# Optimization experiments

Measured on AMD Instinct MI355X. Metric: run time of the kernel, lower is better.

The kernel has to match this reference:

```python
import jax, jax.numpy as jnp
import numpy as np

B, C, L, H = 8, 256, 2048, 4
HD = C // H
LIP = 1.0
EPS = 1e-12
LN_EPS = 1e-5


def setup_inputs() -> dict:
    key = jax.random.key(0)
    ks = jax.random.split(key, 9)
    s = 0.05  # weight init scale
    inp = {"x_in": jax.random.normal(ks[0], (B, C, L), jnp.float32)}
    for i, p in enumerate(["q", "k", "v"]):
        k1, k2 = jax.random.split(ks[1 + i])
        inp[f"{p}_w1"] = jax.random.normal(k1, (C, C), jnp.float32) * s
        inp[f"{p}_b1"] = jnp.zeros((C,), jnp.float32)
        inp[f"{p}_w2"] = jax.random.normal(k2, (C, C), jnp.float32) * s
        inp[f"{p}_b2"] = jnp.zeros((C,), jnp.float32)
    inp["o_w"] = jax.random.normal(ks[4], (C, C), jnp.float32) * s
    inp["o_b"] = jnp.zeros((C,), jnp.float32)
    inp["ln_g"] = jnp.ones((C,), jnp.float32)
    inp["ln_b"] = jnp.zeros((C,), jnp.float32)
    return inp


def _mlp(x, w1, b1, w2, b2):
    # Linear -> exact GELU -> Linear (matches nn.GELU default, erf form)
    return jax.nn.gelu(x @ w1 + b1, approximate=False) @ w2 + b2


def reference(x_in, q_w1, q_b1, q_w2, q_b2, k_w1, k_b1, k_w2, k_b2,
              v_w1, v_b1, v_w2, v_b2, o_w, o_b, ln_g, ln_b):
    x = x_in.transpose(0, 2, 1)  # [B, L, C]

    def heads(t):
        return t.reshape(B, L, H, HD).transpose(0, 2, 1, 3)  # [B, H, L, HD]

    Q = heads(_mlp(x, q_w1, q_b1, q_w2, q_b2))
    K = heads(_mlp(x, k_w1, k_b1, k_w2, k_b2))
    V = heads(_mlp(x, v_w1, v_b1, v_w2, v_b2))

    scores = jnp.einsum('bhqd,bhkd->bhqk', Q, K) / jnp.sqrt(jnp.float32(HD))
    # Lipschitz rescale: divide each score row by its L2 norm
    row_norm = jnp.sqrt(jnp.sum(scores * scores, axis=-1, keepdims=True))
    scores = scores / (row_norm * LIP + EPS)
    attn = jax.nn.softmax(scores, axis=-1)

    out = jnp.einsum('bhqk,bhkd->bhqd', attn, V)  # [B, H, L, HD]
    out = out.transpose(0, 2, 1, 3).reshape(B, L, C)
    out = out @ o_w + o_b

    # LayerNorm over channel dim (torch LN: biased variance, eps=1e-5)
    mu = jnp.mean(out, axis=-1, keepdims=True)
    var = jnp.mean((out - mu) ** 2, axis=-1, keepdims=True)
    out = (out - mu) / jnp.sqrt(var + LN_EPS) * ln_g + ln_b

    out = out.transpose(0, 2, 1)  # [B, C, L]
    return jax.nn.elu(out) + x_in
```

## Files before the change

kernel.cpp:

```cpp
#include <hip/hip_runtime.h>
#include <hip/hip_bf16.h>
#include <cstdint>
#include <cstddef>

#define B_  8
#define C_  256
#define L_  2048
#define H_  4
#define HD_ 64

using short8v = __attribute__((ext_vector_type(8))) short;
using f32x4   = __attribute__((ext_vector_type(4))) float;

__device__ __forceinline__ float gelu_exact(float v) {
  return 0.5f * v * (1.0f + erff(v * 0.70710678118654752440f));
}

__device__ __forceinline__ short f2bf(float v) {
  __hip_bfloat16 h = __float2bfloat16(v);
  return *reinterpret_cast<short*>(&h);
}

__device__ __forceinline__ float bf2f(short s) {
  __hip_bfloat16 h = *reinterpret_cast<__hip_bfloat16*>(&s);
  return __bfloat162float(h);
}

__device__ __forceinline__ void fma16(float (&acc)[4][4], const float4 a, const float4 b) {
  acc[0][0] += a.x * b.x; acc[0][1] += a.x * b.y; acc[0][2] += a.x * b.z; acc[0][3] += a.x * b.w;
  acc[1][0] += a.y * b.x; acc[1][1] += a.y * b.y; acc[1][2] += a.y * b.z; acc[1][3] += a.y * b.w;
  acc[2][0] += a.z * b.x; acc[2][1] += a.z * b.y; acc[2][2] += a.z * b.z; acc[2][3] += a.z * b.w;
  acc[3][0] += a.w * b.x; acc[3][1] += a.w * b.y; acc[3][2] += a.w * b.z; acc[3][3] += a.w * b.w;
}

__global__ __launch_bounds__(256) void k_transpose(const float* __restrict__ x,
                                                   float* __restrict__ Xr) {
  __shared__ float t[32][33];
  const int l0 = blockIdx.x * 32;
  const int c0 = blockIdx.y * 32;
  const int b  = blockIdx.z;
  const int tx = threadIdx.x;
  const int ty = threadIdx.y;
  const float* xp  = x  + (size_t)b * C_ * L_;
  float*       xrp = Xr + (size_t)b * L_ * C_;
#pragma unroll
  for (int i = 0; i < 32; i += 8)
    t[ty + i][tx] = xp[(size_t)(c0 + ty + i) * L_ + (l0 + tx)];
  __syncthreads();
#pragma unroll
  for (int i = 0; i < 32; i += 8)
    xrp[(size_t)(l0 + ty + i) * C_ + (c0 + tx)] = t[tx][ty + i];
}

__global__ __launch_bounds__(256) void k_packw(
    const float* __restrict__ w0, const float* __restrict__ w1,
    const float* __restrict__ w2, const float* __restrict__ w3,
    const float* __restrict__ w4, const float* __restrict__ w5,
    const float* __restrict__ w6,
    short* __restrict__ hi, short* __restrict__ lo) {
  const float* Ws[7] = {w0, w1, w2, w3, w4, w5, w6};
  const int wi = blockIdx.z;
  const float* W = Ws[wi];
  __shared__ float T[32][33];
  const int k0 = blockIdx.x * 32, n0 = blockIdx.y * 32;
  const int tx = threadIdx.x & 31, ty = threadIdx.x >> 5;
#pragma unroll
  for (int i = 0; i < 32; i += 8)
    T[ty + i][tx] = W[(size_t)(k0 + ty + i) * 256 + n0 + tx];
  __syncthreads();
  short* ho = hi + (size_t)wi * 65536;
  short* lp = lo + (size_t)wi * 65536;
#pragma unroll
  for (int i = 0; i < 32; i += 8) {
    float v = T[tx][ty + i];
    short h = f2bf(v);
    float r = v - bf2f(h);
    ho[(size_t)(n0 + ty + i) * 256 + k0 + tx] = h;
    lp[(size_t)(n0 + ty + i) * 256 + k0 + tx] = f2bf(r);
  }
}

__global__ __launch_bounds__(256, 3) void k_gemm_s(
    const float* __restrict__ A, const short* __restrict__ Wth,
    const short* __restrict__ Wtl, const float* __restrict__ bias,
    float* __restrict__ Cout, int actGelu) {
  __shared__ short Ah[2][64 * 32], Al[2][64 * 32];
  __shared__ short Bh[2][128 * 32], Bl[2][128 * 32];
  const int tid  = threadIdx.x;
  const int lane = tid & 63;
  const int w    = tid >> 6;
  const int wm = w & 1, wn = w >> 1;
  const int m0 = blockIdx.x * 64;
  const int n0 = blockIdx.y * 128;
  const int l15 = lane & 15, lg = lane >> 4;

  const int ar  = tid >> 2;
  const int ag  = tid & 3;
  const int br  = tid >> 1;
  const int bg0 = (tid & 1) * 2;

  float4 fA0, fA1;
  short8v rBh0, rBh1, rBl0, rBl1;
  auto gload = [&](int ks) {
    const float* ap = &A[(size_t)(m0 + ar) * 256 + ks * 32 + ag * 8];
    fA0 = *reinterpret_cast<const float4*>(ap);
    fA1 = *reinterpret_cast<const float4*>(ap + 4);
    const short* bph = &Wth[(size_t)(n0 + br) * 256 + ks * 32 + bg0 * 8];
    const short* bpl = &Wtl[(size_t)(n0 + br) * 256 + ks * 32 + bg0 * 8];
    rBh0 = *reinterpret_cast<const short8v*>(bph);
    rBh1 = *reinterpret_cast<const short8v*>(bph + 8);
    rBl0 = *reinterpret_cast<const short8v*>(bpl);
    rBl1 = *reinterpret_cast<const short8v*>(bpl + 8);
  };
  auto lwrite = [&](int buf) {
    float av[8] = {fA0.x, fA0.y, fA0.z, fA0.w, fA1.x, fA1.y, fA1.z, fA1.w};
    short8v h8, l8;
#pragma unroll
    for (int i = 0; i < 8; ++i) {
      short h = f2bf(av[i]);
      h8[i] = h;
      l8[i] = f2bf(av[i] - bf2f(h));
    }
    const int gA = ag ^ (ar & 3);
    *reinterpret_cast<short8v*>(&Ah[buf][ar * 32 + gA * 8]) = h8;
    *reinterpret_cast<short8v*>(&Al[buf][ar * 32 + gA * 8]) = l8;
    const int g0 = bg0 ^ (br & 3);
    const int g1 = (bg0 + 1) ^ (br & 3);
    *reinterpret_cast<short8v*>(&Bh[buf][br * 32 + g0 * 8]) = rBh0;
    *reinterpret_cast<short8v*>(&Bh[buf][br * 32 + g1 * 8]) = rBh1;
    *reinterpret_cast<short8v*>(&Bl[buf][br * 32 + g0 * 8]) = rBl0;
    *reinterpret_cast<short8v*>(&Bl[buf][br * 32 + g1 * 8]) = rBl1;
  };

  const f32x4 z4 = {0.f, 0.f, 0.f, 0.f};
  f32x4 acc[2][4];
#pragma unroll
  for (int s = 0; s < 2; ++s)
#pragma unroll
    for (int nt = 0; nt < 4; ++nt) acc[s][nt] = z4;

  gload(0);
  lwrite(0);
  __syncthreads();

  for (int ks = 0; ks < 8; ++ks) {
    const int cur = ks & 1;
    if (ks < 7) gload(ks + 1);
    short8v a_h[2], a_l[2];
#pragma unroll
    for (int s = 0; s < 2; ++s) {
      const int m = wm * 32 + s * 16 + l15;
      const int g = lg ^ (m & 3);
      a_h[s] = *reinterpret_cast<const short8v*>(&Ah[cur][m * 32 + g * 8]);
      a_l[s] = *reinterpret_cast<const short8v*>(&Al[cur][m * 32 + g * 8]);
    }
#pragma unroll
    for (int nt = 0; nt < 4; ++nt) {
      const int n = wn * 64 + nt * 16 + l15;
      const int g = lg ^ (n & 3);
      short8v b_h = *reinterpret_cast<const short8v*>(&Bh[cur][n * 32 + g * 8]);
      short8v b_l = *reinterpret_cast<const short8v*>(&Bl[cur][n * 32 + g * 8]);
#pragma unroll
      for (int s = 0; s < 2; ++s) {
        acc[s][nt] = __builtin_amdgcn_mfma_f32_16x16x32_bf16(a_h[s], b_h, acc[s][nt], 0, 0, 0);
        acc[s][nt] = __builtin_amdgcn_mfma_f32_16x16x32_bf16(a_h[s], b_l, acc[s][nt], 0, 0, 0);
        acc[s][nt] = __builtin_amdgcn_mfma_f32_16x16x32_bf16(a_l[s], b_h, acc[s][nt], 0, 0, 0);
      }
    }
    if (ks < 7) lwrite(cur ^ 1);
    __syncthreads();
  }

#pragma unroll
  for (int nt = 0; nt < 4; ++nt) {
    const int col = n0 + wn * 64 + nt * 16 + l15;
    const float bv = bias[col];
#pragma unroll
    for (int s = 0; s < 2; ++s)
#pragma unroll
      for (int r = 0; r < 4; ++r) {
        const int row = m0 + wm * 32 + s * 16 + lg * 4 + r;
        float v = acc[s][nt][r] + bv;
        if (actGelu) v = gelu_exact(v);
        Cout[(size_t)row * 256 + col] = v;
      }
  }
}

__global__ __launch_bounds__(256) void k_gram(const float* __restrict__ Kg,
                                              float* __restrict__ Gp) {
  __shared__ float Ks[64][68];
  const int tid = threadIdx.x;
  const int tm = tid >> 4;
  const int tn = tid & 15;
  const int chunk = blockIdx.x;
  const int h = blockIdx.y;
  const int b = blockIdx.z;
  const size_t base = (size_t)b * L_ * C_ + (size_t)h * HD_ + (size_t)chunk * 256 * C_;
  const int lr = tid >> 2;
  const int lf = tid & 3;
  float acc[4][4] = {};
  for (int st = 0; st < 4; ++st) {
    __syncthreads();
#pragma unroll
    for (int i = 0; i < 4; ++i) {
      int fg = lf * 4 + i;
      float4 v = *reinterpret_cast<const float4*>(&Kg[base + (size_t)(st * 64 + lr) * C_ + fg * 4]);
      *reinterpret_cast<float4*>(&Ks[lr][fg * 4]) = v;
    }
    __syncthreads();
#pragma unroll 16
    for (int r = 0; r < 64; ++r) {
      float4 a  = *reinterpret_cast<const float4*>(&Ks[r][tm << 2]);
      float4 b2 = *reinterpret_cast<const float4*>(&Ks[r][tn << 2]);
      fma16(acc, a, b2);
    }
  }
  const int bh = b * H_ + h;
  float* gp = Gp + ((size_t)bh * 8 + chunk) * 4096;
#pragma unroll
  for (int i = 0; i < 4; ++i)
    *reinterpret_cast<float4*>(&gp[((tm << 2) + i) * 64 + (tn << 2)]) =
        make_float4(acc[i][0], acc[i][1], acc[i][2], acc[i][3]);
}

__global__ __launch_bounds__(256) void k_gram_reduce(const float* __restrict__ Gp,
                                                     float* __restrict__ G) {
  const int bh = blockIdx.x;
  const int tid = threadIdx.x;
  for (int t = tid; t < 4096; t += 256) {
    float s = 0.f;
#pragma unroll
    for (int c = 0; c < 8; ++c) s += Gp[((size_t)bh * 8 + c) * 4096 + t];
    G[(size_t)bh * 4096 + t] = s;
  }
}

__global__ __launch_bounds__(256) void k_scale(const float* __restrict__ Qg,
                                               const float* __restrict__ Gm,
                                               float* __restrict__ Scl) {
  __shared__ float QsT[64][68];
  __shared__ float Gs[64][68];
  const int tid = threadIdx.x;
  const int tm = tid >> 4;
  const int tn = tid & 15;
  const int q0 = blockIdx.x * 64;
  const int h  = blockIdx.y;
  const int b  = blockIdx.z;
  const int bh = b * H_ + h;
  const size_t base = (size_t)b * L_ * C_ + (size_t)h * HD_;
  const int lr = tid >> 2;
  const int lf = tid & 3;
#pragma unroll
  for (int i = 0; i < 4; ++i) {
    int fg = lf * 4 + i;
    float4 v = *reinterpret_cast<const float4*>(&Qg[base + (size_t)(q0 + lr) * C_ + fg * 4]);
    QsT[fg * 4 + 0][lr] = v.x;
    QsT[fg * 4 + 1][lr] = v.y;
    QsT[fg * 4 + 2][lr] = v.z;
    QsT[fg * 4 + 3][lr] = v.w;
    float4 g = *reinterpret_cast<const float4*>(&Gm[(size_t)bh * 4096 + lr * 64 + fg * 4]);
    *reinterpret_cast<float4*>(&Gs[lr][fg * 4]) = g;
  }
  __syncthreads();
  float t4[4][4] = {};
#pragma unroll 16
  for (int e = 0; e < 64; ++e) {
    float4 a  = *reinterpret_cast<const float4*>(&QsT[e][tm << 2]);
    float4 b2 = *reinterpret_cast<const float4*>(&Gs[e][tn << 2]);
    fma16(t4, a, b2);
  }
  float r2[4];
#pragma unroll
  for (int i = 0; i < 4; ++i) {
    r2[i] = t4[i][0] * QsT[(tn << 2) + 0][(tm << 2) + i]
          + t4[i][1] * QsT[(tn << 2) + 1][(tm << 2) + i]
          + t4[i][2] * QsT[(tn << 2) + 2][(tm << 2) + i]
          + t4[i][3] * QsT[(tn << 2) + 3][(tm << 2) + i];
#pragma unroll
    for (int o = 8; o; o >>= 1) r2[i] += __shfl_xor(r2[i], o);
  }
  if (tn == 0) {
#pragma unroll
    for (int i = 0; i < 4; ++i) {
      float rr = fmaxf(r2[i], 0.f);
      Scl[(size_t)bh * L_ + q0 + (tm << 2) + i] = 1.0f / (sqrtf(rr) + 8e-12f);
    }
  }
}

__global__ __launch_bounds__(256) void k_pack_qk(const float* __restrict__ Qf,
                                                 const float* __restrict__ Kf,
                                                 short* __restrict__ Qh,
                                                 short* __restrict__ Kh) {
  const int blk = blockIdx.x;
  const int tid = threadIdx.x;
#pragma unroll
  for (int i = 0; i < 16; ++i) {
    int idx = tid + 256 * i;
    int row = idx >> 6;
    int c4  = idx & 63;
    int R = blk * 64 + row;
    int b = R >> 11, l = R & 2047;
    int h = c4 >> 4, d4 = c4 & 15;
    size_t o = ((size_t)(b * H_ + h) * L_ + l) * HD_ + d4 * 4;
    float4 q = *reinterpret_cast<const float4*>(&Qf[(size_t)R * C_ + c4 * 4]);
    float4 k = *reinterpret_cast<const float4*>(&Kf[(size_t)R * C_ + c4 * 4]);
    short4 qs, ks;
    qs.x = f2bf(q.x); qs.y = f2bf(q.y); qs.z = f2bf(q.z); qs.w = f2bf(q.w);
    ks.x = f2bf(k.x); ks.y = f2bf(k.y); ks.z = f2bf(k.z); ks.w = f2bf(k.w);
    *reinterpret_cast<short4*>(&Qh[o]) = qs;
    *reinterpret_cast<short4*>(&Kh[o]) = ks;
  }
}

__global__ __launch_bounds__(256) void k_packt_v(const float* __restrict__ Vf,
                                                 short* __restrict__ Vt) {
  __shared__ float T[64][65];
  const int lt = blockIdx.x;
  const int h = blockIdx.y, b = blockIdx.z;
  const int bh = b * H_ + h;
  const int tid = threadIdx.x;
#pragma unroll
  for (int i = 0; i < 4; ++i) {
    int idx = tid + 256 * i;
    int l = idx >> 4;
    int c4 = idx & 15;
    float4 v = *reinterpret_cast<const float4*>(
        &Vf[(size_t)(b * L_ + lt * 64 + l) * C_ + h * HD_ + c4 * 4]);
    T[l][c4 * 4 + 0] = v.x;
    T[l][c4 * 4 + 1] = v.y;
    T[l][c4 * 4 + 2] = v.z;
    T[l][c4 * 4 + 3] = v.w;
  }
  __syncthreads();
  const int d  = tid >> 2;
  const int ls = (tid & 3) * 16;
#pragma unroll
  for (int i = 0; i < 4; ++i) {
    int l = ls + i * 4;
    short4 s;
    s.x = f2bf(T[l + 0][d]);
    s.y = f2bf(T[l + 1][d]);
    s.z = f2bf(T[l + 2][d]);
    s.w = f2bf(T[l + 3][d]);
    *reinterpret_cast<short4*>(&Vt[((size_t)bh * HD_ + d) * L_ + lt * 64 + l]) = s;
  }
}

__device__ __forceinline__ int swz(int r, int c) {
  return (r * 64 + c) ^ ((r & 7) << 3);
}

__global__ __launch_bounds__(256) void k_attn_mfma(
    const short* __restrict__ Qh, const short* __restrict__ Kh,
    const short* __restrict__ Vt, const float* __restrict__ Scl,
    float* __restrict__ AO) {
  __shared__ short Ks[2][64 * 64];
  __shared__ short Vs[2][64 * 64];
  __shared__ short Ps[4][32 * 64];
  const int tid  = threadIdx.x;
  const int lane = tid & 63;
  const int w    = tid >> 6;
  const int h = blockIdx.y, b = blockIdx.z;
  const int bh = b * H_ + h;
  const size_t hb = (size_t)bh * L_ * HD_;
  const int q0 = blockIdx.x * 128 + w * 32;
  const int l15 = lane & 15;
  const int lg  = lane >> 4;
  const int srow = tid >> 3;
  const int sseg = tid & 7;

  short8v aq[2][2];
#pragma unroll
  for (int sub = 0; sub < 2; ++sub)
#pragma unroll
    for (int ch = 0; ch < 2; ++ch)
      aq[sub][ch] = *reinterpret_cast<const short8v*>(
          &Qh[hb + (size_t)(q0 + sub * 16 + l15) * HD_ + ch * 32 + lg * 8]);

  float sr[2][4];
#pragma unroll
  for (int sub = 0; sub < 2; ++sub)
#pragma unroll
    for (int r = 0; r < 4; ++r)
      sr[sub][r] = Scl[(size_t)bh * L_ + q0 + sub * 16 + lg * 4 + r];

  short8v stK0, stK1, stV0, stV1;
  auto stage_load = [&](int kt) {
    stK0 = *reinterpret_cast<const short8v*>(&Kh[hb + (size_t)(kt * 64 + srow) * HD_ + sseg * 8]);
    stK1 = *reinterpret_cast<const short8v*>(&Kh[hb + (size_t)(kt * 64 + 32 + srow) * HD_ + sseg * 8]);
    stV0 = *reinterpret_cast<const short8v*>(&Vt[hb + (size_t)srow * L_ + kt * 64 + sseg * 8]);
    stV1 = *reinterpret_cast<const short8v*>(&Vt[hb + (size_t)(32 + srow) * L_ + kt * 64 + sseg * 8]);
  };
  auto stage_write = [&](int buf) {
    *reinterpret_cast<short8v*>(&Ks[buf][swz(srow, sseg * 8)]) = stK0;
    *reinterpret_cast<short8v*>(&Ks[buf][swz(32 + srow, sseg * 8)]) = stK1;
    *reinterpret_cast<short8v*>(&Vs[buf][swz(srow, sseg * 8)]) = stV0;
    *reinterpret_cast<short8v*>(&Vs[buf][swz(32 + srow, sseg * 8)]) = stV1;
  };

  const f32x4 z4 = {0.f, 0.f, 0.f, 0.f};
  float lsum[2][4] = {};
  f32x4 oacc[2][4];
#pragma unroll
  for (int s = 0; s < 2; ++s)
#pragma unroll
    for (int d = 0; d < 4; ++d) oacc[s][d] = z4;

  stage_load(0);
  stage_write(0);
  __syncthreads();

  for (int kt = 0; kt < 32; ++kt) {
    const int cur = kt & 1;
    if (kt < 31) stage_load(kt + 1);

    f32x4 sacc[2][4];
#pragma unroll
    for (int s = 0; s < 2; ++s)
#pragma unroll
      for (int nt = 0; nt < 4; ++nt) sacc[s][nt] = z4;
#pragma unroll
    for (int nt = 0; nt < 4; ++nt) {
      short8v kb0 = *reinterpret_cast<const short8v*>(&Ks[cur][swz(nt * 16 + l15, lg * 8)]);
      short8v kb1 = *reinterpret_cast<const short8v*>(&Ks[cur][swz(nt * 16 + l15, 32 + lg * 8)]);
#pragma unroll
      for (int sub = 0; sub < 2; ++sub) {
        sacc[sub][nt] = __builtin_amdgcn_mfma_f32_16x16x32_bf16(aq[sub][0], kb0, sacc[sub][nt], 0, 0, 0);
        sacc[sub][nt] = __builtin_amdgcn_mfma_f32_16x16x32_bf16(aq[sub][1], kb1, sacc[sub][nt], 0, 0, 0);
      }
    }

#pragma unroll
    for (int sub = 0; sub < 2; ++sub)
#pragma unroll
      for (int nt = 0; nt < 4; ++nt)
#pragma unroll
        for (int r = 0; r < 4; ++r) {
          float p = __expf(sacc[sub][nt][r] * sr[sub][r]);
          lsum[sub][r] += p;
          Ps[w][swz(sub * 16 + lg * 4 + r, nt * 16 + l15)] = f2bf(p);
        }
    asm volatile("s_waitcnt lgkmcnt(0)");
    __builtin_amdgcn_sched_barrier(0);

    short8v pa[2][2];
#pragma unroll
    for (int sub = 0; sub < 2; ++sub) {
      pa[sub][0] = *reinterpret_cast<const short8v*>(&Ps[w][swz(sub * 16 + l15, lg * 8)]);
      pa[sub][1] = *reinterpret_cast<const short8v*>(&Ps[w][swz(sub * 16 + l15, 32 + lg * 8)]);
    }
#pragma unroll
    for (int dt = 0; dt < 4; ++dt) {
      short8v vb0 = *reinterpret_cast<const short8v*>(&Vs[cur][swz(dt * 16 + l15, lg * 8)]);
      short8v vb1 = *reinterpret_cast<const short8v*>(&Vs[cur][swz(dt * 16 + l15, 32 + lg * 8)]);
#pragma unroll
      for (int sub = 0; sub < 2; ++sub) {
        oacc[sub][dt] = __builtin_amdgcn_mfma_f32_16x16x32_bf16(pa[sub][0], vb0, oacc[sub][dt], 0, 0, 0);
        oacc[sub][dt] = __builtin_amdgcn_mfma_f32_16x16x32_bf16(pa[sub][1], vb1, oacc[sub][dt], 0, 0, 0);
      }
    }
    __syncthreads();
    if (kt < 31) {
      stage_write(cur ^ 1);
      __syncthreads();
    }
  }

#pragma unroll
  for (int sub = 0; sub < 2; ++sub)
#pragma unroll
    for (int r = 0; r < 4; ++r) {
#pragma unroll
      for (int o = 8; o; o >>= 1) lsum[sub][r] += __shfl_xor(lsum[sub][r], o);
    }

#pragma unroll
  for (int sub = 0; sub < 2; ++sub)
#pragma unroll
    for (int r = 0; r < 4; ++r) {
      const float inv = 1.0f / lsum[sub][r];
      const int q = q0 + sub * 16 + lg * 4 + r;
#pragma unroll
      for (int dt = 0; dt < 4; ++dt)
        AO[(size_t)(b * L_ + q) * C_ + h * HD_ + dt * 16 + l15] = oacc[sub][dt][r] * inv;
    }
}

__global__ __launch_bounds__(256) void k_ln(const float* __restrict__ PO,
                                            const float* __restrict__ x,
                                            const float* __restrict__ g,
                                            const float* __restrict__ bta,
                                            float* __restrict__ out) {
  __shared__ float buf[32][257];
  __shared__ float mu_s[32], rs_s[32];
  __shared__ float gs[256], bs[256];
  const int b  = blockIdx.y;
  const int l0 = blockIdx.x * 32;
  const int tid = threadIdx.x;
  gs[tid] = g[tid];
  bs[tid] = bta[tid];
#pragma unroll 8
  for (int r = 0; r < 32; ++r)
    buf[r][tid] = PO[((size_t)b * L_ + l0 + r) * C_ + tid];
  __syncthreads();
  {
    const int r  = tid >> 3;
    const int c0 = tid & 7;
    float s1 = 0.f;
#pragma unroll
    for (int i = 0; i < 32; ++i) s1 += buf[r][c0 + (i << 3)];
#pragma unroll
    for (int o = 4; o; o >>= 1) s1 += __shfl_xor(s1, o);
    float mu = s1 * (1.0f / 256.0f);
    float s2 = 0.f;
#pragma unroll
    for (int i = 0; i < 32; ++i) {
      float dv = buf[r][c0 + (i << 3)] - mu;
      s2 += dv * dv;
    }
#pragma unroll
    for (int o = 4; o; o >>= 1) s2 += __shfl_xor(s2, o);
    if (c0 == 0) {
      mu_s[r] = mu;
      rs_s[r] = rsqrtf(s2 * (1.0f / 256.0f) + 1e-5f);
    }
  }
  __syncthreads();
  const int tl = tid & 31;
  const int tc = tid >> 5;
  const float mu = mu_s[tl];
  const float rs = rs_s[tl];
#pragma unroll 8
  for (int c = tc; c < 256; c += 8) {
    float y = (buf[tl][c] - mu) * rs * gs[c] + bs[c];
    float e = (y > 0.f) ? y : (__expf(y) - 1.0f);
    size_t idx = ((size_t)b * C_ + c) * L_ + l0 + tl;
    out[idx] = e + x[idx];
  }
}

extern "C" void kernel_launch(void* const* d_in, const int* in_sizes, int n_in,
                              void* d_out, int out_size, void* d_ws, size_t ws_size,
                              hipStream_t stream) {
  const float* x_in = (const float*)d_in[0];
  const float* q_w1 = (const float*)d_in[1];
  const float* q_b1 = (const float*)d_in[2];
  const float* q_w2 = (const float*)d_in[3];
  const float* q_b2 = (const float*)d_in[4];
  const float* k_w1 = (const float*)d_in[5];
  const float* k_b1 = (const float*)d_in[6];
  const float* k_w2 = (const float*)d_in[7];
  const float* k_b2 = (const float*)d_in[8];
  const float* v_w1 = (const float*)d_in[9];
  const float* v_b1 = (const float*)d_in[10];
  const float* v_w2 = (const float*)d_in[11];
  const float* v_b2 = (const float*)d_in[12];
  const float* o_w  = (const float*)d_in[13];
  const float* o_b  = (const float*)d_in[14];
  const float* ln_g = (const float*)d_in[15];
  const float* ln_b = (const float*)d_in[16];
  float* out = (float*)d_out;
  float* ws  = (float*)d_ws;

  const size_t NB = (size_t)B_ * L_ * C_;
  float* Xr = ws;
  float* Hb = ws + NB;
  float* Qb = ws + 2 * NB;
  float* Kb = ws + 3 * NB;
  float* Gp = ws + 4 * NB;
  float* G  = Gp + (size_t)32 * 8 * 4096;
  float* Scl = G + (size_t)32 * 4096;
  short* Vt  = (short*)(Scl + (size_t)32 * 2048);
  short* Whi = Vt + (size_t)32 * HD_ * L_;
  short* Wlo = Whi + (size_t)7 * 65536;
  float* Vb = Xr;
  short* Qh = (short*)Hb;
  short* Kh = (short*)(Hb + NB / 2);
  float* AO = Kb;
  float* PO = Qb;

  dim3 ggrid(B_ * L_ / 64, C_ / 128);

  k_packw<<<dim3(8, 8, 7), 256, 0, stream>>>(q_w1, q_w2, k_w1, k_w2, v_w1, v_w2, o_w, Whi, Wlo);
  k_transpose<<<dim3(L_ / 32, C_ / 32, B_), dim3(32, 8), 0, stream>>>(x_in, Xr);

  const size_t WN = 65536;
  k_gemm_s<<<ggrid, 256, 0, stream>>>(Xr, Whi + 0 * WN, Wlo + 0 * WN, q_b1, Hb, 1);
  k_gemm_s<<<ggrid, 256, 0, stream>>>(Hb, Whi + 1 * WN, Wlo + 1 * WN, q_b2, Qb, 0);
  k_gemm_s<<<ggrid, 256, 0, stream>>>(Xr, Whi + 2 * WN, Wlo + 2 * WN, k_b1, Hb, 1);
  k_gemm_s<<<ggrid, 256, 0, stream>>>(Hb, Whi + 3 * WN, Wlo + 3 * WN, k_b2, Kb, 0);
  k_gemm_s<<<ggrid, 256, 0, stream>>>(Xr, Whi + 4 * WN, Wlo + 4 * WN, v_b1, Hb, 1);
  k_gemm_s<<<ggrid, 256, 0, stream>>>(Hb, Whi + 5 * WN, Wlo + 5 * WN, v_b2, Vb, 0);

  k_gram<<<dim3(8, H_, B_), 256, 0, stream>>>(Kb, Gp);
  k_gram_reduce<<<dim3(32), 256, 0, stream>>>(Gp, G);
  k_scale<<<dim3(L_ / 64, H_, B_), 256, 0, stream>>>(Qb, G, Scl);

  k_pack_qk<<<dim3(B_ * L_ / 64), 256, 0, stream>>>(Qb, Kb, Qh, Kh);
  k_packt_v<<<dim3(L_ / 64, H_, B_), 256, 0, stream>>>(Vb, Vt);

  k_attn_mfma<<<dim3(L_ / 128, H_, B_), 256, 0, stream>>>(Qh, Kh, Vt, Scl, AO);

  k_gemm_s<<<ggrid, 256, 0, stream>>>(AO, Whi + 6 * WN, Wlo + 6 * WN, o_b, PO, 0);

  k_ln<<<dim3(L_ / 32, B_), 256, 0, stream>>>(PO, x_in, ln_g, ln_b, out);
}
```

Before: 318.3 us.

## Store intermediates as pre-split bf16 hi/lo pairs and drop the separate Q/K packing pass

```diff
diff --git a/kernel.cpp b/kernel.cpp
--- a/kernel.cpp
+++ b/kernel.cpp
@@ -33,23 +33,28 @@
   acc[3][0] += a.w * b.x; acc[3][1] += a.w * b.y; acc[3][2] += a.w * b.z; acc[3][3] += a.w * b.w;
 }
 
-__global__ __launch_bounds__(256) void k_transpose(const float* __restrict__ x,
-                                                   float* __restrict__ Xr) {
+__global__ __launch_bounds__(256) void k_transpose_s(const float* __restrict__ x,
+                                                     short* __restrict__ Xh,
+                                                     short* __restrict__ Xl) {
   __shared__ float t[32][33];
   const int l0 = blockIdx.x * 32;
   const int c0 = blockIdx.y * 32;
   const int b  = blockIdx.z;
   const int tx = threadIdx.x;
   const int ty = threadIdx.y;
-  const float* xp  = x  + (size_t)b * C_ * L_;
-  float*       xrp = Xr + (size_t)b * L_ * C_;
+  const float* xp = x + (size_t)b * C_ * L_;
 #pragma unroll
   for (int i = 0; i < 32; i += 8)
     t[ty + i][tx] = xp[(size_t)(c0 + ty + i) * L_ + (l0 + tx)];
   __syncthreads();
 #pragma unroll
-  for (int i = 0; i < 32; i += 8)
-    xrp[(size_t)(l0 + ty + i) * C_ + (c0 + tx)] = t[tx][ty + i];
+  for (int i = 0; i < 32; i += 8) {
+    float v = t[tx][ty + i];
+    short hi = f2bf(v);
+    size_t o = ((size_t)b * L_ + l0 + ty + i) * C_ + c0 + tx;
+    Xh[o] = hi;
+    Xl[o] = f2bf(v - bf2f(hi));
+  }
 }
 
 __global__ __launch_bounds__(256) void k_packw(
@@ -80,64 +85,48 @@
   }
 }
 
-__global__ __launch_bounds__(256, 3) void k_gemm_s(
-    const float* __restrict__ A, const short* __restrict__ Wth,
-    const short* __restrict__ Wtl, const float* __restrict__ bias,
-    float* __restrict__ Cout, int actGelu) {
-  __shared__ short Ah[2][64 * 32], Al[2][64 * 32];
-  __shared__ short Bh[2][128 * 32], Bl[2][128 * 32];
+__global__ __launch_bounds__(256, 4) void k_gemm_p(
+    const short* __restrict__ Ahp, const short* __restrict__ Alp,
+    const short* __restrict__ Whp, const short* __restrict__ Wlp,
+    const float* __restrict__ bias,
+    short* __restrict__ outH, short* __restrict__ outL,
+    float* __restrict__ outF,
+    int actGelu, int wantLo, int wantF32) {
+  __shared__ __attribute__((aligned(16))) short Ah[2][64 * 32], Al[2][64 * 32];
+  __shared__ __attribute__((aligned(16))) short Bh[2][64 * 32], Bl[2][64 * 32];
   const int tid  = threadIdx.x;
   const int lane = tid & 63;
   const int w    = tid >> 6;
   const int wm = w & 1, wn = w >> 1;
   const int m0 = blockIdx.x * 64;
-  const int n0 = blockIdx.y * 128;
+  const int n0 = blockIdx.y * 64;
   const int l15 = lane & 15, lg = lane >> 4;
-
-  const int ar  = tid >> 2;
-  const int ag  = tid & 3;
-  const int br  = tid >> 1;
-  const int bg0 = (tid & 1) * 2;
-
-  float4 fA0, fA1;
-  short8v rBh0, rBh1, rBl0, rBl1;
+  const int ar = tid >> 2;
+  const int ag = tid & 3;
+
+  short8v rah, ral, rbh, rbl;
   auto gload = [&](int ks) {
-    const float* ap = &A[(size_t)(m0 + ar) * 256 + ks * 32 + ag * 8];
-    fA0 = *reinterpret_cast<const float4*>(ap);
-    fA1 = *reinterpret_cast<const float4*>(ap + 4);
-    const short* bph = &Wth[(size_t)(n0 + br) * 256 + ks * 32 + bg0 * 8];
-    const short* bpl = &Wtl[(size_t)(n0 + br) * 256 + ks * 32 + bg0 * 8];
-    rBh0 = *reinterpret_cast<const short8v*>(bph);
-    rBh1 = *reinterpret_cast<const short8v*>(bph + 8);
-    rBl0 = *reinterpret_cast<const short8v*>(bpl);
-    rBl1 = *reinterpret_cast<const short8v*>(bpl + 8);
+    const size_t ao = (size_t)(m0 + ar) * 256 + ks * 32 + ag * 8;
+    rah = *reinterpret_cast<const short8v*>(&Ahp[ao]);
+    ral = *reinterpret_cast<const short8v*>(&Alp[ao]);
+    const size_t bo = (size_t)(n0 + ar) * 256 + ks * 32 + ag * 8;
+    rbh = *reinterpret_cast<const short8v*>(&Whp[bo]);
+    rbl = *reinterpret_cast<const short8v*>(&Wlp[bo]);
   };
   auto lwrite = [&](int buf) {
-    float av[8] = {fA0.x, fA0.y, fA0.z, fA0.w, fA1.x, fA1.y, fA1.z, fA1.w};
-    short8v h8, l8;
-#pragma unroll
-    for (int i = 0; i < 8; ++i) {
-      short h = f2bf(av[i]);
-      h8[i] = h;
-      l8[i] = f2bf(av[i] - bf2f(h));
-    }
-    const int gA = ag ^ (ar & 3);
-    *reinterpret_cast<short8v*>(&Ah[buf][ar * 32 + gA * 8]) = h8;
-    *reinterpret_cast<short8v*>(&Al[buf][ar * 32 + gA * 8]) = l8;
-    const int g0 = bg0 ^ (br & 3);
-    const int g1 = (bg0 + 1) ^ (br & 3);
-    *reinterpret_cast<short8v*>(&Bh[buf][br * 32 + g0 * 8]) = rBh0;
-    *reinterpret_cast<short8v*>(&Bh[buf][br * 32 + g1 * 8]) = rBh1;
-    *reinterpret_cast<short8v*>(&Bl[buf][br * 32 + g0 * 8]) = rBl0;
-    *reinterpret_cast<short8v*>(&Bl[buf][br * 32 + g1 * 8]) = rBl1;
+    const int g = ag ^ (ar & 3);
+    *reinterpret_cast<short8v*>(&Ah[buf][ar * 32 + g * 8]) = rah;
+    *reinterpret_cast<short8v*>(&Al[buf][ar * 32 + g * 8]) = ral;
+    *reinterpret_cast<short8v*>(&Bh[buf][ar * 32 + g * 8]) = rbh;
+    *reinterpret_cast<short8v*>(&Bl[buf][ar * 32 + g * 8]) = rbl;
   };
 
   const f32x4 z4 = {0.f, 0.f, 0.f, 0.f};
-  f32x4 acc[2][4];
+  f32x4 acc[2][2];
 #pragma unroll
   for (int s = 0; s < 2; ++s)
 #pragma unroll
-    for (int nt = 0; nt < 4; ++nt) acc[s][nt] = z4;
+    for (int t = 0; t < 2; ++t) acc[s][t] = z4;
 
   gload(0);
   lwrite(0);
@@ -146,7 +135,7 @@
   for (int ks = 0; ks < 8; ++ks) {
     const int cur = ks & 1;
     if (ks < 7) gload(ks + 1);
-    short8v a_h[2], a_l[2];
+    short8v a_h[2], a_l[2], b_h[2], b_l[2];
 #pragma unroll
     for (int s = 0; s < 2; ++s) {
       const int m = wm * 32 + s * 16 + l15;
@@ -155,39 +144,48 @@
       a_l[s] = *reinterpret_cast<const short8v*>(&Al[cur][m * 32 + g * 8]);
     }
 #pragma unroll
-    for (int nt = 0; nt < 4; ++nt) {
-      const int n = wn * 64 + nt * 16 + l15;
+    for (int t = 0; t < 2; ++t) {
+      const int n = wn * 32 + t * 16 + l15;
       const int g = lg ^ (n & 3);
-      short8v b_h = *reinterpret_cast<const short8v*>(&Bh[cur][n * 32 + g * 8]);
-      short8v b_l = *reinterpret_cast<const short8v*>(&Bl[cur][n * 32 + g * 8]);
-#pragma unroll
-      for (int s = 0; s < 2; ++s) {
-        acc[s][nt] = __builtin_amdgcn_mfma_f32_16x16x32_bf16(a_h[s], b_h, acc[s][nt], 0, 0, 0);
-        acc[s][nt] = __builtin_amdgcn_mfma_f32_16x16x32_bf16(a_h[s], b_l, acc[s][nt], 0, 0, 0);
-        acc[s][nt] = __builtin_amdgcn_mfma_f32_16x16x32_bf16(a_l[s], b_h, acc[s][nt], 0, 0, 0);
+      b_h[t] = *reinterpret_cast<const short8v*>(&Bh[cur][n * 32 + g * 8]);
+      b_l[t] = *reinterpret_cast<const short8v*>(&Bl[cur][n * 32 + g * 8]);
+    }
+#pragma unroll
+    for (int s = 0; s < 2; ++s)
+#pragma unroll
+      for (int t = 0; t < 2; ++t) {
+        acc[s][t] = __builtin_amdgcn_mfma_f32_16x16x32_bf16(a_h[s], b_h[t], acc[s][t], 0, 0, 0);
+        acc[s][t] = __builtin_amdgcn_mfma_f32_16x16x32_bf16(a_h[s], b_l[t], acc[s][t], 0, 0, 0);
+        acc[s][t] = __builtin_amdgcn_mfma_f32_16x16x32_bf16(a_l[s], b_h[t], acc[s][t], 0, 0, 0);
       }
-    }
     if (ks < 7) lwrite(cur ^ 1);
     __syncthreads();
   }
 
 #pragma unroll
-  for (int nt = 0; nt < 4; ++nt) {
-    const int col = n0 + wn * 64 + nt * 16 + l15;
+  for (int t = 0; t < 2; ++t) {
+    const int col = n0 + wn * 32 + t * 16 + l15;
     const float bv = bias[col];
 #pragma unroll
     for (int s = 0; s < 2; ++s)
 #pragma unroll
       for (int r = 0; r < 4; ++r) {
         const int row = m0 + wm * 32 + s * 16 + lg * 4 + r;
-        float v = acc[s][nt][r] + bv;
+        float v = acc[s][t][r] + bv;
         if (actGelu) v = gelu_exact(v);
-        Cout[(size_t)row * 256 + col] = v;
+        const size_t o = (size_t)row * 256 + col;
+        if (wantF32) {
+          outF[o] = v;
+        } else {
+          short hv = f2bf(v);
+          outH[o] = hv;
+          if (wantLo) outL[o] = f2bf(v - bf2f(hv));
+        }
       }
   }
 }
 
-__global__ __launch_bounds__(256) void k_gram(const float* __restrict__ Kg,
+__global__ __launch_bounds__(256) void k_gram(const short* __restrict__ Kp,
                                               float* __restrict__ Gp) {
   __shared__ float Ks[64][68];
   const int tid = threadIdx.x;
@@ -205,8 +203,11 @@
 #pragma unroll
     for (int i = 0; i < 4; ++i) {
       int fg = lf * 4 + i;
-      float4 v = *reinterpret_cast<const float4*>(&Kg[base + (size_t)(st * 64 + lr) * C_ + fg * 4]);
-      *reinterpret_cast<float4*>(&Ks[lr][fg * 4]) = v;
+      short4 s4 = *reinterpret_cast<const short4*>(&Kp[base + (size_t)(st * 64 + lr) * C_ + fg * 4]);
+      Ks[lr][fg * 4 + 0] = bf2f(s4.x);
+      Ks[lr][fg * 4 + 1] = bf2f(s4.y);
+      Ks[lr][fg * 4 + 2] = bf2f(s4.z);
+      Ks[lr][fg * 4 + 3] = bf2f(s4.w);
     }
     __syncthreads();
 #pragma unroll 16
@@ -236,7 +237,7 @@
   }
 }
 
-__global__ __launch_bounds__(256) void k_scale(const float* __restrict__ Qg,
+__global__ __launch_bounds__(256) void k_scale(const short* __restrict__ Qp,
                                                const float* __restrict__ Gm,
                                                float* __restrict__ Scl) {
   __shared__ float QsT[64][68];
@@ -254,11 +255,11 @@
 #pragma unroll
   for (int i = 0; i < 4; ++i) {
     int fg = lf * 4 + i;
-    float4 v = *reinterpret_cast<const float4*>(&Qg[base + (size_t)(q0 + lr) * C_ + fg * 4]);
-    QsT[fg * 4 + 0][lr] = v.x;
-    QsT[fg * 4 + 1][lr] = v.y;
-    QsT[fg * 4 + 2][lr] = v.z;
-    QsT[fg * 4 + 3][lr] = v.w;
+    short4 s4 = *reinterpret_cast<const short4*>(&Qp[base + (size_t)(q0 + lr) * C_ + fg * 4]);
+    QsT[fg * 4 + 0][lr] = bf2f(s4.x);
+    QsT[fg * 4 + 1][lr] = bf2f(s4.y);
+    QsT[fg * 4 + 2][lr] = bf2f(s4.z);
+    QsT[fg * 4 + 3][lr] = bf2f(s4.w);
     float4 g = *reinterpret_cast<const float4*>(&Gm[(size_t)bh * 4096 + lr * 64 + fg * 4]);
     *reinterpret_cast<float4*>(&Gs[lr][fg * 4]) = g;
   }
@@ -289,34 +290,9 @@
   }
 }
 
-__global__ __launch_bounds__(256) void k_pack_qk(const float* __restrict__ Qf,
-                                                 const float* __restrict__ Kf,
-                                                 short* __restrict__ Qh,
-                                                 short* __restrict__ Kh) {
-  const int blk = blockIdx.x;
-  const int tid = threadIdx.x;
-#pragma unroll
-  for (int i = 0; i < 16; ++i) {
-    int idx = tid + 256 * i;
-    int row = idx >> 6;
-    int c4  = idx & 63;
-    int R = blk * 64 + row;
-    int b = R >> 11, l = R & 2047;
-    int h = c4 >> 4, d4 = c4 & 15;
-    size_t o = ((size_t)(b * H_ + h) * L_ + l) * HD_ + d4 * 4;
-    float4 q = *reinterpret_cast<const float4*>(&Qf[(size_t)R * C_ + c4 * 4]);
-    float4 k = *reinterpret_cast<const float4*>(&Kf[(size_t)R * C_ + c4 * 4]);
-    short4 qs, ks;
-    qs.x = f2bf(q.x); qs.y = f2bf(q.y); qs.z = f2bf(q.z); qs.w = f2bf(q.w);
-    ks.x = f2bf(k.x); ks.y = f2bf(k.y); ks.z = f2bf(k.z); ks.w = f2bf(k.w);
-    *reinterpret_cast<short4*>(&Qh[o]) = qs;
-    *reinterpret_cast<short4*>(&Kh[o]) = ks;
-  }
-}
-
-__global__ __launch_bounds__(256) void k_packt_v(const float* __restrict__ Vf,
+__global__ __launch_bounds__(256) void k_packt_v(const short* __restrict__ Vp,
                                                  short* __restrict__ Vt) {
-  __shared__ float T[64][65];
+  __shared__ __attribute__((aligned(16))) short T[64][68];
   const int lt = blockIdx.x;
   const int h = blockIdx.y, b = blockIdx.z;
   const int bh = b * H_ + h;
@@ -326,24 +302,21 @@
     int idx = tid + 256 * i;
     int l = idx >> 4;
     int c4 = idx & 15;
-    float4 v = *reinterpret_cast<const float4*>(
-        &Vf[(size_t)(b * L_ + lt * 64 + l) * C_ + h * HD_ + c4 * 4]);
-    T[l][c4 * 4 + 0] = v.x;
-    T[l][c4 * 4 + 1] = v.y;
-    T[l][c4 * 4 + 2] = v.z;
-    T[l][c4 * 4 + 3] = v.w;
-  }
-  __syncthreads();
-  const int d  = tid >> 2;
-  const int ls = (tid & 3) * 16;
+    short4 v = *reinterpret_cast<const short4*>(
+        &Vp[(size_t)(b * L_ + lt * 64 + l) * C_ + h * HD_ + c4 * 4]);
+    *reinterpret_cast<short4*>(&T[l][c4 * 4]) = v;
+  }
+  __syncthreads();
+  const int d = tid >> 2;
+  const int j = tid & 3;
 #pragma unroll
   for (int i = 0; i < 4; ++i) {
-    int l = ls + i * 4;
+    int l = j * 4 + i * 16;
     short4 s;
-    s.x = f2bf(T[l + 0][d]);
-    s.y = f2bf(T[l + 1][d]);
-    s.z = f2bf(T[l + 2][d]);
-    s.w = f2bf(T[l + 3][d]);
+    s.x = T[l + 0][d];
+    s.y = T[l + 1][d];
+    s.z = T[l + 2][d];
+    s.w = T[l + 3][d];
     *reinterpret_cast<short4*>(&Vt[((size_t)bh * HD_ + d) * L_ + lt * 64 + l]) = s;
   }
 }
@@ -353,19 +326,24 @@
 }
 
 __global__ __launch_bounds__(256) void k_attn_mfma(
-    const short* __restrict__ Qh, const short* __restrict__ Kh,
+    const short* __restrict__ Qp, const short* __restrict__ Kp,
     const short* __restrict__ Vt, const float* __restrict__ Scl,
-    float* __restrict__ AO) {
-  __shared__ short Ks[2][64 * 64];
-  __shared__ short Vs[2][64 * 64];
-  __shared__ short Ps[4][32 * 64];
+    short* __restrict__ AOh, short* __restrict__ AOl) {
+  __shared__ __attribute__((aligned(16))) short Ks[2][64 * 64];
+  __shared__ __attribute__((aligned(16))) short Vs[2][64 * 64];
+  __shared__ __attribute__((aligned(16))) short Ps[4][32 * 64];
   const int tid  = threadIdx.x;
   const int lane = tid & 63;
   const int w    = tid >> 6;
-  const int h = blockIdx.y, b = blockIdx.z;
-  const int bh = b * H_ + h;
-  const size_t hb = (size_t)bh * L_ * HD_;
-  const int q0 = blockIdx.x * 128 + w * 32;
+  const int u   = blockIdx.x;
+  const int xcd = u & 7;
+  const int qi  = (u >> 3) & 15;
+  const int g   = u >> 7;
+  const int bh  = g * 8 + xcd;
+  const int b = bh >> 2, h = bh & 3;
+  const size_t rowbase = (size_t)b * L_ * C_ + (size_t)h * HD_;
+  const size_t vtb = (size_t)bh * HD_ * L_;
+  const int q0 = qi * 128 + w * 32;
   const int l15 = lane & 15;
   const int lg  = lane >> 4;
   const int srow = tid >> 3;
@@ -377,21 +355,19 @@
 #pragma unroll
     for (int ch = 0; ch < 2; ++ch)
       aq[sub][ch] = *reinterpret_cast<const short8v*>(
-          &Qh[hb + (size_t)(q0 + sub * 16 + l15) * HD_ + ch * 32 + lg * 8]);
-
-  float sr[2][4];
+          &Qp[rowbase + (size_t)(q0 + sub * 16 + l15) * C_ + ch * 32 + lg * 8]);
+
+  float sr[2];
 #pragma unroll
   for (int sub = 0; sub < 2; ++sub)
-#pragma unroll
-    for (int r = 0; r < 4; ++r)
-      sr[sub][r] = Scl[(size_t)bh * L_ + q0 + sub * 16 + lg * 4 + r];
+    sr[sub] = Scl[(size_t)bh * L_ + q0 + sub * 16 + l15];
 
   short8v stK0, stK1, stV0, stV1;
   auto stage_load = [&](int kt) {
-    stK0 = *reinterpret_cast<const short8v*>(&Kh[hb + (size_t)(kt * 64 + srow) * HD_ + sseg * 8]);
-    stK1 = *reinterpret_cast<const short8v*>(&Kh[hb + (size_t)(kt * 64 + 32 + srow) * HD_ + sseg * 8]);
-    stV0 = *reinterpret_cast<const short8v*>(&Vt[hb + (size_t)srow * L_ + kt * 64 + sseg * 8]);
-    stV1 = *reinterpret_cast<const short8v*>(&Vt[hb + (size_t)(32 + srow) * L_ + kt * 64 + sseg * 8]);
+    stK0 = *reinterpret_cast<const short8v*>(&Kp[rowbase + (size_t)(kt * 64 + srow) * C_ + sseg * 8]);
+    stK1 = *reinterpret_cast<const short8v*>(&Kp[rowbase + (size_t)(kt * 64 + 32 + srow) * C_ + sseg * 8]);
+    stV0 = *reinterpret_cast<const short8v*>(&Vt[vtb + (size_t)srow * L_ + kt * 64 + sseg * 8]);
+    stV1 = *reinterpret_cast<const short8v*>(&Vt[vtb + (size_t)(32 + srow) * L_ + kt * 64 + sseg * 8]);
   };
   auto stage_write = [&](int buf) {
     *reinterpret_cast<short8v*>(&Ks[buf][swz(srow, sseg * 8)]) = stK0;
@@ -401,7 +377,7 @@
   };
 
   const f32x4 z4 = {0.f, 0.f, 0.f, 0.f};
-  float lsum[2][4] = {};
+  float lsum[2] = {0.f, 0.f};
   f32x4 oacc[2][4];
 #pragma unroll
   for (int s = 0; s < 2; ++s)
@@ -427,21 +403,25 @@
       short8v kb1 = *reinterpret_cast<const short8v*>(&Ks[cur][swz(nt * 16 + l15, 32 + lg * 8)]);
 #pragma unroll
       for (int sub = 0; sub < 2; ++sub) {
-        sacc[sub][nt] = __builtin_amdgcn_mfma_f32_16x16x32_bf16(aq[sub][0], kb0, sacc[sub][nt], 0, 0, 0);
-        sacc[sub][nt] = __builtin_amdgcn_mfma_f32_16x16x32_bf16(aq[sub][1], kb1, sacc[sub][nt], 0, 0, 0);
+        sacc[sub][nt] = __builtin_amdgcn_mfma_f32_16x16x32_bf16(kb0, aq[sub][0], sacc[sub][nt], 0, 0, 0);
+        sacc[sub][nt] = __builtin_amdgcn_mfma_f32_16x16x32_bf16(kb1, aq[sub][1], sacc[sub][nt], 0, 0, 0);
       }
     }
 
 #pragma unroll
     for (int sub = 0; sub < 2; ++sub)
 #pragma unroll
-      for (int nt = 0; nt < 4; ++nt)
-#pragma unroll
-        for (int r = 0; r < 4; ++r) {
-          float p = __expf(sacc[sub][nt][r] * sr[sub][r]);
-          lsum[sub][r] += p;
-          Ps[w][swz(sub * 16 + lg * 4 + r, nt * 16 + l15)] = f2bf(p);
-        }
+      for (int nt = 0; nt < 4; ++nt) {
+        float p0 = __expf(sacc[sub][nt][0] * sr[sub]);
+        float p1 = __expf(sacc[sub][nt][1] * sr[sub]);
+        float p2 = __expf(sacc[sub][nt][2] * sr[sub]);
+        float p3 = __expf(sacc[sub][nt][3] * sr[sub]);
+        lsum[sub] += (p0 + p1) + (p2 + p3);
+        unsigned int w0 = (unsigned short)f2bf(p0) | ((unsigned int)(unsigned short)f2bf(p1) << 16);
+        unsigned int w1 = (unsigned short)f2bf(p2) | ((unsigned int)(unsigned short)f2bf(p3) << 16);
+        uint2 pk; pk.x = w0; pk.y = w1;
+        *reinterpret_cast<uint2*>(&Ps[w][swz(sub * 16 + l15, nt * 16 + lg * 4)]) = pk;
+      }
     asm volatile("s_waitcnt lgkmcnt(0)");
     __builtin_amdgcn_sched_barrier(0);
 
@@ -469,22 +449,25 @@
   }
 
 #pragma unroll
+  for (int sub = 0; sub < 2; ++sub) {
+    lsum[sub] += __shfl_xor(lsum[sub], 16);
+    lsum[sub] += __shfl_xor(lsum[sub], 32);
+  }
+
+#pragma unroll
   for (int sub = 0; sub < 2; ++sub)
 #pragma unroll
     for (int r = 0; r < 4; ++r) {
-#pragma unroll
-      for (int o = 8; o; o >>= 1) lsum[sub][r] += __shfl_xor(lsum[sub][r], o);
-    }
-
-#pragma unroll
-  for (int sub = 0; sub < 2; ++sub)
-#pragma unroll
-    for (int r = 0; r < 4; ++r) {
-      const float inv = 1.0f / lsum[sub][r];
+      const float inv = 1.0f / __shfl(lsum[sub], lg * 4 + r);
       const int q = q0 + sub * 16 + lg * 4 + r;
 #pragma unroll
-      for (int dt = 0; dt < 4; ++dt)
-        AO[(size_t)(b * L_ + q) * C_ + h * HD_ + dt * 16 + l15] = oacc[sub][dt][r] * inv;
+      for (int dt = 0; dt < 4; ++dt) {
+        float v = oacc[sub][dt][r] * inv;
+        short hv = f2bf(v);
+        const size_t o = rowbase + (size_t)q * C_ + dt * 16 + l15;
+        AOh[o] = hv;
+        AOl[o] = f2bf(v - bf2f(hv));
+      }
     }
 }
 
@@ -562,48 +545,46 @@
   const float* ln_g = (const float*)d_in[15];
   const float* ln_b = (const float*)d_in[16];
   float* out = (float*)d_out;
-  float* ws  = (float*)d_ws;
 
   const size_t NB = (size_t)B_ * L_ * C_;
-  float* Xr = ws;
-  float* Hb = ws + NB;
-  float* Qb = ws + 2 * NB;
-  float* Kb = ws + 3 * NB;
-  float* Gp = ws + 4 * NB;
+  short* Xh = (short*)d_ws;
+  short* Xl = Xh + NB;
+  short* Hh = Xl + NB;
+  short* Hl = Hh + NB;
+  short* Qp = Hl + NB;
+  short* Kp = Qp + NB;
+  short* Vp = Kp + NB;
+  float* Gp = (float*)(Vp + NB);
   float* G  = Gp + (size_t)32 * 8 * 4096;
   float* Scl = G + (size_t)32 * 4096;
-  short* Vt  = (short*)(Scl + (size_t)32 * 2048);
-  short* Whi = Vt + (size_t)32 * HD_ * L_;
+  short* Whi = (short*)(Scl + (size_t)32 * 2048);
   short* Wlo = Whi + (size_t)7 * 65536;
-  float* Vb = Xr;
-  short* Qh = (short*)Hb;
-  short* Kh = (short*)(Hb + NB / 2);
-  float* AO = Kb;
-  float* PO = Qb;
-
-  dim3 ggrid(B_ * L_ / 64, C_ / 128);
+  float* PO  = (float*)Xh;
+  short* AOh = Hh;
+  short* Vt  = Hl;
+  short* AOl = Vp;
+
+  const size_t WN = 65536;
+  dim3 gg(256, 4);
 
   k_packw<<<dim3(8, 8, 7), 256, 0, stream>>>(q_w1, q_w2, k_w1, k_w2, v_w1, v_w2, o_w, Whi, Wlo);
-  k_transpose<<<dim3(L_ / 32, C_ / 32, B_), dim3(32, 8), 0, stream>>>(x_in, Xr);
-
-  const size_t WN = 65536;
-  k_gemm_s<<<ggrid, 256, 0, stream>>>(Xr, Whi + 0 * WN, Wlo + 0 * WN, q_b1, Hb, 1);
-  k_gemm_s<<<ggrid, 256, 0, stream>>>(Hb, Whi + 1 * WN, Wlo + 1 * WN, q_b2, Qb, 0);
-  k_gemm_s<<<ggrid, 256, 0, stream>>>(Xr, Whi + 2 * WN, Wlo + 2 * WN, k_b1, Hb, 1);
-  k_gemm_s<<<ggrid, 256, 0, stream>>>(Hb, Whi + 3 * WN, Wlo + 3 * WN, k_b2, Kb, 0);
-  k_gemm_s<<<ggrid, 256, 0, stream>>>(Xr, Whi + 4 * WN, Wlo + 4 * WN, v_b1, Hb, 1);
-  k_gemm_s<<<ggrid, 256, 0, stream>>>(Hb, Whi + 5 * WN, Wlo + 5 * WN, v_b2, Vb, 0);
-
-  k_gram<<<dim3(8, H_, B_), 256, 0, stream>>>(Kb, Gp);
+  k_transpose_s<<<dim3(L_ / 32, C_ / 32, B_), dim3(32, 8), 0, stream>>>(x_in, Xh, Xl);
+
+  k_gemm_p<<<gg, 256, 0, stream>>>(Xh, Xl, Whi + 0 * WN, Wlo + 0 * WN, q_b1, Hh, Hl, nullptr, 1, 1, 0);
+  k_gemm_p<<<gg, 256, 0, stream>>>(Hh, Hl, Whi + 1 * WN, Wlo + 1 * WN, q_b2, Qp, nullptr, nullptr, 0, 0, 0);
+  k_gemm_p<<<gg, 256, 0, stream>>>(Xh, Xl, Whi + 2 * WN, Wlo + 2 * WN, k_b1, Hh, Hl, nullptr, 1, 1, 0);
+  k_gemm_p<<<gg, 256, 0, stream>>>(Hh, Hl, Whi + 3 * WN, Wlo + 3 * WN, k_b2, Kp, nullptr, nullptr, 0, 0, 0);
+  k_gemm_p<<<gg, 256, 0, stream>>>(Xh, Xl, Whi + 4 * WN, Wlo + 4 * WN, v_b1, Hh, Hl, nullptr, 1, 1, 0);
+  k_gemm_p<<<gg, 256, 0, stream>>>(Hh, Hl, Whi + 5 * WN, Wlo + 5 * WN, v_b2, Vp, nullptr, nullptr, 0, 0, 0);
+
+  k_gram<<<dim3(8, H_, B_), 256, 0, stream>>>(Kp, Gp);
   k_gram_reduce<<<dim3(32), 256, 0, stream>>>(Gp, G);
-  k_scale<<<dim3(L_ / 64, H_, B_), 256, 0, stream>>>(Qb, G, Scl);
-
-  k_pack_qk<<<dim3(B_ * L_ / 64), 256, 0, stream>>>(Qb, Kb, Qh, Kh);
-  k_packt_v<<<dim3(L_ / 64, H_, B_), 256, 0, stream>>>(Vb, Vt);
-
-  k_attn_mfma<<<dim3(L_ / 128, H_, B_), 256, 0, stream>>>(Qh, Kh, Vt, Scl, AO);
-
-  k_gemm_s<<<ggrid, 256, 0, stream>>>(AO, Whi + 6 * WN, Wlo + 6 * WN, o_b, PO, 0);
+  k_scale<<<dim3(L_ / 64, H_, B_), 256, 0, stream>>>(Qp, G, Scl);
+  k_packt_v<<<dim3(L_ / 64, H_, B_), 256, 0, stream>>>(Vp, Vt);
+
+  k_attn_mfma<<<dim3(512), 256, 0, stream>>>(Qp, Kp, Vt, Scl, AOh, AOl);
+
+  k_gemm_p<<<gg, 256, 0, stream>>>(AOh, AOl, Whi + 6 * WN, Wlo + 6 * WN, o_b, nullptr, nullptr, PO, 0, 0, 1);
 
   k_ln<<<dim3(L_ / 32, B_), 256, 0, stream>>>(PO, x_in, ln_g, ln_b, out);
 }
```

Result: faster. 304.5 us (-4.4%).
